# Performance work log

Measured on AMD Instinct MI355X. Metric: run time of the kernel, lower is better.

## Reference

```python
import jax, jax.numpy as jnp
import numpy as np

NX, NY, NM, NDT, NU, ND = 128, 64, 32, 32, 32, 32
N_STEPS, B, TP = 1024, 128, 64


def _spectral_weight(U, sig, V, smin, smax):
    # W = U @ diag(sigma_clamped) @ V with sigma in [smin, smax];
    # spectral (orthogonality) error penalizes non-orthogonal U, V.
    s = smin + (smax - smin) * jax.nn.sigmoid(sig)
    nin, nout = U.shape[0], V.shape[0]
    k = s.shape[0]
    Sigma = jnp.zeros((nin, nout), U.dtype).at[jnp.arange(k), jnp.arange(k)].set(s)
    W = U @ Sigma @ V
    err = jnp.mean((U @ U.T - jnp.eye(nin, dtype=U.dtype)) ** 2) \
        + jnp.mean((V @ V.T - jnp.eye(nout, dtype=V.dtype)) ** 2)
    return W, err


def _pf_weight(w, scal, smin, smax):
    # Perron-Frobenius interval weight: column-stochastic (softmax over rows)
    # scaled elementwise into [smin, smax].
    s = smax - (smax - smin) * jax.nn.sigmoid(scal)
    return s * jax.nn.softmax(w, axis=0)


def setup_inputs() -> dict:
    key = jax.random.key(0)
    ks = jax.random.split(key, 20)
    f = lambda i, sh, sc=1.0: jax.random.normal(ks[i], sh, jnp.float32) * sc
    u = lambda i, sh: jax.random.uniform(ks[i], sh, jnp.float32)
    inp = {
        # forward data args
        "Ym": f(0, (TP, B, NY)),
        "M_flow": u(1, (N_STEPS, B, NM)),
        "DT": u(2, (N_STEPS, B, NDT)),
        "D": u(3, (N_STEPS, B, ND)),
        "XMIN": jnp.zeros((N_STEPS, B, NX), jnp.float32),
        "XMAX": jnp.ones((N_STEPS, B, NX), jnp.float32),
        "UMIN": jnp.zeros((N_STEPS, B, NU), jnp.float32),
        "UMAX": jnp.ones((N_STEPS, B, NU), jnp.float32),
        # learned parameters
        "x0_correct": jnp.zeros((1, NX), jnp.float32),
        "U_A": f(4, (NX, NX), 0.1), "sig_A": u(5, (NX,)), "V_A": f(6, (NX, NX), 0.1),
        "U_C": f(7, (NX, NX), 0.1), "sig_C": u(8, (NY,)), "V_C": f(9, (NY, NY), 0.1),
        "w_E": u(10, (ND, NX)), "s_E": u(11, (ND, NX)),
        "w_B": f(12, (NU, NX), 0.1),
        "W_hf": f(13, (NU, NM, NDT), 0.1),
        "W_ih": f(14, (NY, NX), 0.1), "W_hh": f(15, (NX, NX), 0.1),
        # non-trainable buffers
        "dxmin": -0.5 * jnp.ones((1, NX), jnp.float32),
        "dxmax": 0.5 * jnp.ones((1, NX), jnp.float32),
    }
    return inp


def _forward(Ym, M_flow, DT, D, XMIN, XMAX, UMIN, UMAX, x0_correct,
             U_A, sig_A, V_A, U_C, sig_C, V_C, w_E, s_E, w_B, W_hf,
             W_ih, W_hh, dxmin, dxmax):
    W_A, errA = _spectral_weight(U_A, sig_A, V_A, 0.1, 0.9)   # state transition, sigma in [0.1,0.9]
    W_C, errC = _spectral_weight(U_C, sig_C, V_C, 0.9, 1.0)   # output map, sigma in [0.9,1]
    W_E = _pf_weight(w_E, s_E, 0.05, 1.0)                      # disturbance map
    W_Bpos = jax.nn.relu(w_B)                                  # non-negative input map
    spect_err = errA + errC

    # RNN state estimator over past observations; x0 = last hidden output
    def rnn_step(h, y_t):
        h = jax.nn.gelu(y_t @ W_ih + h @ W_hh)
        return h, None
    h0 = jnp.zeros((Ym.shape[1], W_ih.shape[1]), Ym.dtype)
    x0, _ = jax.lax.scan(rnn_step, h0, Ym)

    def step(x, ins):
        m, dT, d, xmin, xmax, umin, umax = ins
        x_prev = x
        xc = x + x0_correct
        u = jnp.einsum('bi,oij,bj->bo', m, W_hf, dT)   # bilinear heat flow
        Bu = u @ W_Bpos
        Ed = d @ W_E
        x_new = xc @ W_A + Bu + Ed
        y = x_new @ W_C
        sxmin = jax.nn.relu(xmin - x_new)
        sxmax = jax.nn.relu(x_new - xmax)
        sumin = jax.nn.relu(umin - u)
        sumax = jax.nn.relu(u - umax)
        dx_x = x_new - x_prev
        dx_u = jax.nn.relu(dxmin - Bu) + jax.nn.relu(Bu - dxmax)
        dx_d = jax.nn.relu(dxmin - Ed) + jax.nn.relu(Ed - dxmax)
        return x_new, (x_new, y, u, sxmin, sxmax, sumin, sumax, dx_x, dx_u, dx_d)

    _, outs = jax.lax.scan(step, x0, (M_flow, DT, D, XMIN, XMAX, UMIN, UMAX))
    X, Y, U, Sxmin, Sxmax, Sumin, Sumax, Sdx_x, Sdx_u, Sdx_d = outs
    SpectErr = jnp.full((M_flow.shape[0],), spect_err)
    return (X, Y, U, Sxmin, Sxmax, Sumin, Sumax, Sdx_x, Sdx_u, Sdx_d, SpectErr)


def reference(Ym, M_flow, DT, D, XMIN, XMAX, UMIN, UMAX, x0_correct,
              U_A, sig_A, V_A, U_C, sig_C, V_C, w_E, s_E, w_B, W_hf,
              W_ih, W_hh, dxmin, dxmax):
    return _forward(Ym, M_flow, DT, D, XMIN, XMAX, UMIN, UMAX, x0_correct,
                    U_A, sig_A, V_A, U_C, sig_C, V_C, w_E, s_E, w_B, W_hf,
                    W_ih, W_hh, dxmin, dxmax)
```

## Files before the change

kernel.cpp:

```cpp
#include <hip/hip_runtime.h>
#include <math.h>


#define OUT_X      0
#define OUT_Y      16777216
#define OUT_U      25165824
#define OUT_SXMIN  29360128
#define OUT_SXMAX  46137344
#define OUT_SUMIN  62914560
#define OUT_SUMAX  67108864
#define OUT_SDXX   71303168
#define OUT_SDXU   88080384
#define OUT_SDXD   104857600
#define OUT_SPECT  121634816

#define WS_WA     0
#define WS_APOW   65536
#define WS_WC     589824
#define WS_WB     606208
#define WS_WE     614400
#define WS_WHF    622592
#define WS_R      688128
#define WS_ERRP   688640
#define WS_Z      1048576
#define WS_C      5242880
#define WS_XLOC   38797312

#define XSTR 136

typedef _Float16 half8  __attribute__((ext_vector_type(8)));
typedef _Float16 half4v __attribute__((ext_vector_type(4)));
typedef float    floatx4 __attribute__((ext_vector_type(4)));

#define MFMA16(a,b,c) __builtin_amdgcn_mfma_f32_16x16x32_f16((a),(b),(c),0,0,0)

__device__ __forceinline__ float sigm(float x){ return 1.0f/(1.0f+expf(-x)); }
__device__ __forceinline__ float gelu_t(float x){
  float u = 0.7978845608028654f*(x + 0.044715f*x*x*x);
  return 0.5f*x*(1.0f+tanhf(u));
}
__device__ __forceinline__ half8 ldg8h(const float* p){
  const floatx4* p4 = (const floatx4*)p;
  floatx4 a = p4[0], b = p4[1];
  half8 r;
  r[0]=(_Float16)a[0]; r[1]=(_Float16)a[1]; r[2]=(_Float16)a[2]; r[3]=(_Float16)a[3];
  r[4]=(_Float16)b[0]; r[5]=(_Float16)b[1]; r[6]=(_Float16)b[2]; r[7]=(_Float16)b[3];
  return r;
}
__device__ __forceinline__ half8 lds8h(const float* p){
  half8 r;
  #pragma unroll
  for (int e=0;e<8;e++) r[e] = (_Float16)p[e];
  return r;
}
__device__ __forceinline__ floatx4 h4f4(half4v h){
  floatx4 f; f[0]=(float)h[0]; f[1]=(float)h[1]; f[2]=(float)h[2]; f[3]=(float)h[3]; return f;
}
__device__ __forceinline__ half4v f4h4(floatx4 f){
  half4v h; h[0]=(_Float16)f[0]; h[1]=(_Float16)f[1]; h[2]=(_Float16)f[2]; h[3]=(_Float16)f[3]; return h;
}

__global__ __launch_bounds__(256) void k1_weights(
    const float* __restrict__ U_A, const float* __restrict__ sig_A, const float* __restrict__ V_A,
    const float* __restrict__ U_C, const float* __restrict__ sig_C, const float* __restrict__ V_C,
    const float* __restrict__ w_E, const float* __restrict__ s_E,  const float* __restrict__ w_B,
    const float* __restrict__ W_hf, char* __restrict__ ws)
{
  int tid = threadIdx.x, bid = blockIdx.x;
  __shared__ float sA[128];
  __shared__ float sC[64];
  __shared__ float red[256];
  if (tid < 128) sA[tid] = 0.1f + 0.8f*sigm(sig_A[tid]);
  else if (tid < 192) sC[tid-128] = 0.9f + 0.1f*sigm(sig_C[tid-128]);
  __syncthreads();

  float*     wa  = (float*)(ws + WS_WA);
  _Float16*  ap1 = (_Float16*)(ws + WS_APOW);
  _Float16*  wc  = (_Float16*)(ws + WS_WC);
  _Float16*  wb  = (_Float16*)(ws + WS_WB);
  _Float16*  we  = (_Float16*)(ws + WS_WE);
  _Float16*  whf = (_Float16*)(ws + WS_WHF);
  float*     errp= (float*)(ws + WS_ERRP);

  {
    int e = bid*256 + tid;
    int i = e >> 7, j = e & 127;
    float acc = 0.f;
    for (int k=0;k<128;k++) acc += U_A[i*128+k]*sA[k]*V_A[k*128+j];
    wa[i*128+j] = acc;
    ap1[j*128+i] = (_Float16)acc;
  }
  if (bid < 16){
    #pragma unroll
    for (int rep=0;rep<2;rep++){
      int e = bid*512 + rep*256 + tid;
      int i = e >> 6, n = e & 63;
      float acc = 0.f;
      for (int k=0;k<64;k++) acc += U_C[i*128+k]*sC[k]*V_C[k*64+n];
      wc[n*128+i] = (_Float16)acc;
    }
  } else if (bid == 16){
    if (tid < 128){
      int j = tid;
      float mx = -1e30f;
      for (int i=0;i<32;i++) mx = fmaxf(mx, w_E[i*128+j]);
      float ex[32]; float sm = 0.f;
      for (int i=0;i<32;i++){ ex[i] = expf(w_E[i*128+j]-mx); sm += ex[i]; }
      for (int i=0;i<32;i++){
        float s = 1.0f - 0.95f*sigm(s_E[i*128+j]);
        we[j*32+i] = (_Float16)(s*ex[i]/sm);
      }
    }
  } else if (bid == 17){
    if (tid < 128){
      int n = tid;
      for (int k=0;k<32;k++) wb[n*32+k] = (_Float16)fmaxf(w_B[k*128+n], 0.f);
    }
  } else if (bid == 18){
    for (int rep=0;rep<128;rep++){
      int e = rep*256 + tid;
      int o = e >> 10, i = (e>>5)&31, j = e & 31;
      whf[i*1024 + o*32 + j] = (_Float16)W_hf[e];
    }
  }

  float part = 0.f;
  for (int dl = tid; dl < 832; dl += 256){
    int d = bid*832 + dl;
    const float* Mp; int i,j,K,ld; float nrm;
    if (d < 16384){ Mp=U_A; int dd=d;        i=dd>>7; j=dd&127; K=128; ld=128; nrm=16384.f; }
    else if (d < 32768){ Mp=V_A; int dd=d-16384; i=dd>>7; j=dd&127; K=128; ld=128; nrm=16384.f; }
    else if (d < 49152){ Mp=U_C; int dd=d-32768; i=dd>>7; j=dd&127; K=128; ld=128; nrm=16384.f; }
    else { Mp=V_C; int dd=d-49152; i=dd>>6; j=dd&63; K=64; ld=64; nrm=4096.f; }
    float s = 0.f;
    for (int k=0;k<K;k++) s += Mp[i*ld+k]*Mp[j*ld+k];
    float cdf = s - (i==j ? 1.f : 0.f);
    part += cdf*cdf/nrm;
  }
  red[tid] = part;
  __syncthreads();
  for (int off=128; off>0; off>>=1){
    if (tid < off) red[tid] += red[tid+off];
    __syncthreads();
  }
  if (tid == 0) errp[bid] = red[0];
}

__global__ __launch_bounds__(256) void k1b_finalize(
    const float* __restrict__ x0c, char* __restrict__ ws, float* __restrict__ out)
{
  int tid = threadIdx.x;
  const float* errp = (const float*)(ws + WS_ERRP);
  const float* wa   = (const float*)(ws + WS_WA);
  float*       rws  = (float*)(ws + WS_R);
  __shared__ float red[64];
  if (tid < 64) red[tid] = errp[tid];
  __syncthreads();
  if (tid == 0){
    float s = 0.f;
    for (int i=0;i<64;i++) s += red[i];
    red[0] = s;
  }
  __syncthreads();
  float spect = red[0];
  for (int r = tid; r < 1024; r += 256) out[OUT_SPECT + r] = spect;
  if (tid < 128){
    float a = 0.f;
    for (int k=0;k<128;k++) a += x0c[k]*wa[k*128+tid];
    rws[tid] = a;
  }
}

__global__ __launch_bounds__(128,1) void k2_seq(
    const float* __restrict__ Ym, const float* __restrict__ W_ih, const float* __restrict__ W_hh,
    char* __restrict__ ws)
{
  int tid = threadIdx.x, bid = blockIdx.x;
  __shared__ _Float16 xl2[2][64*XSTR];
  __shared__ float yb[64];
  __shared__ float hb[128];

  if (bid < 128){
    int b = bid, j = tid;
    float wih[64], whh[128];
    #pragma unroll
    for (int k=0;k<64;k++)  wih[k] = W_ih[k*128+j];
    #pragma unroll
    for (int k=0;k<128;k++) whh[k] = W_hh[k*128+j];
    hb[j] = 0.f;
    __syncthreads();
    for (int t=0;t<64;t++){
      if (tid < 64) yb[tid] = Ym[(t*128+b)*64 + tid];
      __syncthreads();
      float a = 0.f;
      #pragma unroll
      for (int k=0;k<64;k++)  a += yb[k]*wih[k];
      #pragma unroll
      for (int k=0;k<128;k++) a += hb[k]*whh[k];
      __syncthreads();
      hb[j] = gelu_t(a);
      __syncthreads();
    }
    float* z0 = (float*)(ws + WS_Z);
    z0[b*128 + j] = hb[j];
  } else {
    int wave = tid>>6, lane = tid&63, l15 = lane&15, q = lane>>4;
    const float*    wa = (const float*)(ws + WS_WA);
    const _Float16* a1 = (const _Float16*)(ws + WS_APOW);
    half8 af[4][4];
    #pragma unroll
    for (int mt=0;mt<4;mt++)
      #pragma unroll
      for (int kt=0;kt<4;kt++)
        af[mt][kt] = ldg8h(wa + (wave*64+mt*16+l15)*128 + kt*32 + q*8);
    for (int p=2;p<=16;p++){
      _Float16* dst = (_Float16*)(ws + WS_APOW + (p-1)*32768);
      for (int nt=0;nt<8;nt++){
        floatx4 acc[4];
        #pragma unroll
        for (int mt=0;mt<4;mt++){ acc[mt][0]=0.f; acc[mt][1]=0.f; acc[mt][2]=0.f; acc[mt][3]=0.f; }
        #pragma unroll
        for (int kt=0;kt<4;kt++){
          half8 bf = *(const half8*)(a1 + (nt*16+l15)*128 + kt*32 + q*8);
          #pragma unroll
          for (int mt=0;mt<4;mt++) acc[mt] = MFMA16(af[mt][kt], bf, acc[mt]);
        }
        #pragma unroll
        for (int mt=0;mt<4;mt++){
          half4v hv = f4h4(acc[mt]);
          int mg = wave*64 + mt*16;
          *(half4v*)(dst + (nt*16+l15)*128 + mg + q*4) = hv;
          #pragma unroll
          for (int r=0;r<4;r++) xl2[wave][(mt*16+q*4+r)*XSTR + nt*16+l15] = hv[r];
        }
      }
      #pragma unroll
      for (int mt=0;mt<4;mt++)
        #pragma unroll
        for (int kt=0;kt<4;kt++)
          af[mt][kt] = *(const half8*)(&xl2[wave][(mt*16+l15)*XSTR + kt*32 + q*8]);
    }
  }
}

__global__ __launch_bounds__(256,2) void k3_forcing(
    const float* __restrict__ Mf, const float* __restrict__ pDT, const float* __restrict__ pD,
    const float* __restrict__ pUMIN, const float* __restrict__ pUMAX,
    const float* __restrict__ pdxmin, const float* __restrict__ pdxmax,
    char* __restrict__ ws, float* __restrict__ out)
{
  int t = blockIdx.x, tid = threadIdx.x;
  int wave = tid>>6, lane = tid&63, l15 = lane&15, q = lane>>4;
  __shared__ float mls[128*33];
  __shared__ float uls[4][32*34];
  __shared__ float rls[128], dmn[128], dmx[128];

  const float* rws = (const float*)(ws + WS_R);
  for (int e=tid; e<4096; e+=256){
    float v = Mf[t*4096 + e];
    mls[(e>>5)*33 + (e&31)] = v;
  }
  if (tid < 128){ rls[tid]=rws[tid]; dmn[tid]=pdxmin[tid]; dmx[tid]=pdxmax[tid]; }
  __syncthreads();

  int b0 = wave*32 + l15;
  int b1 = wave*32 + 16 + l15;
  half8 dtf0 = ldg8h(pDT + t*4096 + b0*32 + q*8);
  half8 dtf1 = ldg8h(pDT + t*4096 + b1*32 + q*8);
  half8 ddf0 = ldg8h(pD  + t*4096 + b0*32 + q*8);
  half8 ddf1 = ldg8h(pD  + t*4096 + b1*32 + q*8);

  const _Float16* whf = (const _Float16*)(ws + WS_WHF);
  floatx4 u00,u01,u10,u11;
  u00[0]=u00[1]=u00[2]=u00[3]=0.f; u01=u00; u10=u00; u11=u00;
  for (int i=0;i<32;i++){
    _Float16 m0 = (_Float16)mls[b0*33 + i];
    _Float16 m1 = (_Float16)mls[b1*33 + i];
    half8 a0, a1;
    #pragma unroll
    for (int e=0;e<8;e++){ a0[e] = dtf0[e]*m0; a1[e] = dtf1[e]*m1; }
    half8 bo0 = *(const half8*)(whf + i*1024 + l15*32      + q*8);
    half8 bo1 = *(const half8*)(whf + i*1024 + (16+l15)*32 + q*8);
    u00 = MFMA16(a0, bo0, u00); u01 = MFMA16(a0, bo1, u01);
    u10 = MFMA16(a1, bo0, u10); u11 = MFMA16(a1, bo1, u11);
  }
  #pragma unroll
  for (int mt=0;mt<2;mt++){
    #pragma unroll
    for (int nto=0;nto<2;nto++){
      floatx4 uacc = mt ? (nto?u11:u10) : (nto?u01:u00);
      #pragma unroll
      for (int r=0;r<4;r++){
        int b = wave*32 + mt*16 + q*4 + r;
        int o = nto*16 + l15;
        int ub = t*4096 + b*32 + o;
        float uv = uacc[r];
        out[OUT_U + ub] = uv;
        out[OUT_SUMIN + ub] = fmaxf(pUMIN[ub]-uv, 0.f);
        out[OUT_SUMAX + ub] = fmaxf(uv-pUMAX[ub], 0.f);
        uls[wave][(mt*16+q*4+r)*34 + o] = uv;
      }
    }
  }
  half8 uf0 = lds8h(&uls[wave][(l15)*34 + q*8]);
  half8 uf1 = lds8h(&uls[wave][(16+l15)*34 + q*8]);

  const _Float16* wb = (const _Float16*)(ws + WS_WB);
  const _Float16* we = (const _Float16*)(ws + WS_WE);
  _Float16* cws = (_Float16*)(ws + WS_C);
  for (int nt=0; nt<8; nt++){
    half8 wbf = *(const half8*)(wb + (nt*16+l15)*32 + q*8);
    half8 wef = *(const half8*)(we + (nt*16+l15)*32 + q*8);
    floatx4 zz; zz[0]=zz[1]=zz[2]=zz[3]=0.f;
    floatx4 bu0=MFMA16(uf0, wbf, zz), bu1=MFMA16(uf1, wbf, zz);
    floatx4 ed0=MFMA16(ddf0, wef, zz), ed1=MFMA16(ddf1, wef, zz);
    int col = nt*16 + l15;
    float dn = dmn[col], dxv = dmx[col], rv = rls[col];
    #pragma unroll
    for (int mt=0;mt<2;mt++){
      floatx4 bu = mt?bu1:bu0, ed = mt?ed1:ed0;
      half4v cp;
      #pragma unroll
      for (int r=0;r<4;r++){
        int b = wave*32 + mt*16 + q*4 + r;
        int base = t*16384 + b*128 + col;
        float buv = bu[r], edv = ed[r];
        out[OUT_SDXU + base] = fmaxf(dn-buv,0.f) + fmaxf(buv-dxv,0.f);
        out[OUT_SDXD + base] = fmaxf(dn-edv,0.f) + fmaxf(edv-dxv,0.f);
        cp[r] = (_Float16)(rv + buv + edv);
      }
      *(half4v*)(cws + (((t*8 + (wave*2+mt))*8 + nt)<<8) + lane*4) = cp;
    }
  }
}

__global__ __launch_bounds__(256,1) void k5a_pass1(char* __restrict__ ws)
{
  int tid = threadIdx.x;
  int wave = tid>>6, lane = tid&63, l15 = lane&15, q = lane>>4;
  int chunk = blockIdx.x >> 1, half = blockIdx.x & 1;
  int mt_g = half*4 + wave;
  const _Float16* a1   = (const _Float16*)(ws + WS_APOW);
  const _Float16* cws  = (const _Float16*)(ws + WS_C);
  _Float16*       xloc = (_Float16*)(ws + WS_XLOC);
  __shared__ _Float16 xl[4][16*XSTR];

  half8 bf[8][4];
  #pragma unroll
  for (int nt=0;nt<8;nt++)
    #pragma unroll
    for (int kt=0;kt<4;kt++)
      bf[nt][kt] = *(const half8*)(a1 + (nt*16+l15)*128 + kt*32 + q*8);
  half8 af[4] = {};

  for (int s=0;s<16;s++){
    int t = chunk*16 + s;
    floatx4 acc[8];
    #pragma unroll
    for (int nt=0;nt<8;nt++){
      half4v cv = *(const half4v*)(cws + (((t*8+mt_g)*8+nt)<<8) + lane*4);
      acc[nt] = h4f4(cv);
    }
    #pragma unroll
    for (int kt=0;kt<4;kt++)
      #pragma unroll
      for (int nt=0;nt<8;nt++)
        acc[nt] = MFMA16(af[kt], bf[nt][kt], acc[nt]);
    #pragma unroll
    for (int nt=0;nt<8;nt++){
      half4v hv = f4h4(acc[nt]);
      *(half4v*)(xloc + (((t*8+mt_g)*8+nt)<<8) + lane*4) = hv;
      #pragma unroll
      for (int r=0;r<4;r++) xl[wave][(q*4+r)*XSTR + nt*16+l15] = hv[r];
    }
    #pragma unroll
    for (int kt=0;kt<4;kt++)
      af[kt] = *(const half8*)(&xl[wave][l15*XSTR + kt*32 + q*8]);
  }
}

__global__ __launch_bounds__(64,1) void k5b_boundary(char* __restrict__ ws)
{
  int lane = threadIdx.x, l15 = lane&15, q = lane>>4;
  int mt_g = blockIdx.x;
  const _Float16* a16  = (const _Float16*)(ws + WS_APOW + 15*32768);
  const _Float16* xloc = (const _Float16*)(ws + WS_XLOC);
  float*          z    = (float*)(ws + WS_Z);
  __shared__ _Float16 xl[16*XSTR];

  half8 bf[8][4];
  #pragma unroll
  for (int nt=0;nt<8;nt++)
    #pragma unroll
    for (int kt=0;kt<4;kt++)
      bf[nt][kt] = *(const half8*)(a16 + (nt*16+l15)*128 + kt*32 + q*8);
  half8 af[4];
  #pragma unroll
  for (int kt=0;kt<4;kt++)
    af[kt] = ldg8h(z + (mt_g*16+l15)*128 + kt*32 + q*8);

  for (int c=0;c<63;c++){
    int t = c*16 + 15;
    floatx4 acc[8];
    #pragma unroll
    for (int nt=0;nt<8;nt++){
      half4v hv = *(const half4v*)(xloc + (((t*8+mt_g)*8+nt)<<8) + lane*4);
      acc[nt] = h4f4(hv);
    }
    #pragma unroll
    for (int kt=0;kt<4;kt++)
      #pragma unroll
      for (int nt=0;nt<8;nt++)
        acc[nt] = MFMA16(af[kt], bf[nt][kt], acc[nt]);
    #pragma unroll
    for (int nt=0;nt<8;nt++){
      #pragma unroll
      for (int r=0;r<4;r++){
        int b = mt_g*16 + q*4 + r;
        z[(c+1)*16384 + b*128 + nt*16+l15] = acc[nt][r];
        xl[(q*4+r)*XSTR + nt*16+l15] = (_Float16)acc[nt][r];
      }
    }
    #pragma unroll
    for (int kt=0;kt<4;kt++)
      af[kt] = *(const half8*)(&xl[l15*XSTR + kt*32 + q*8]);
  }
}

__global__ __launch_bounds__(256,2) void k6_epilogue(
    const float* __restrict__ pXMIN, const float* __restrict__ pXMAX,
    char* __restrict__ ws, float* __restrict__ out)
{
  int t = blockIdx.x, tid = threadIdx.x;
  int wave = tid>>6, lane = tid&63, l15 = lane&15, q = lane>>4;
  int c = t>>4, k = t&15;
  __shared__ _Float16 xl[4][32*XSTR];

  const float*    zp   = (const float*)(ws + WS_Z) + c*16384;
  const _Float16* xloc = (const _Float16*)(ws + WS_XLOC);
  const _Float16* ap1  = (const _Float16*)(ws + WS_APOW + k*32768);
  const _Float16* ap0  = (const _Float16*)(ws + WS_APOW + (k-1)*32768);

  half8 zf[2][4];
  #pragma unroll
  for (int mt=0;mt<2;mt++)
    #pragma unroll
    for (int kt=0;kt<4;kt++)
      zf[mt][kt] = ldg8h(zp + (wave*32+mt*16+l15)*128 + kt*32 + q*8);

  for (int nt=0;nt<8;nt++){
    int col = nt*16 + l15;
    floatx4 xt[2], xm[2];
    #pragma unroll
    for (int mt=0;mt<2;mt++)
      xt[mt] = h4f4(*(const half4v*)(xloc + (((t*8 + wave*2+mt)*8 + nt)<<8) + lane*4));
    #pragma unroll
    for (int kt=0;kt<4;kt++){
      half8 b1 = *(const half8*)(ap1 + (nt*16+l15)*128 + kt*32 + q*8);
      #pragma unroll
      for (int mt=0;mt<2;mt++) xt[mt] = MFMA16(zf[mt][kt], b1, xt[mt]);
    }
    if (k > 0){
      #pragma unroll
      for (int mt=0;mt<2;mt++)
        xm[mt] = h4f4(*(const half4v*)(xloc + ((((t-1)*8 + wave*2+mt)*8 + nt)<<8) + lane*4));
      #pragma unroll
      for (int kt=0;kt<4;kt++){
        half8 b0 = *(const half8*)(ap0 + (nt*16+l15)*128 + kt*32 + q*8);
        #pragma unroll
        for (int mt=0;mt<2;mt++) xm[mt] = MFMA16(zf[mt][kt], b0, xm[mt]);
      }
    } else {
      #pragma unroll
      for (int mt=0;mt<2;mt++)
        #pragma unroll
        for (int r=0;r<4;r++)
          xm[mt][r] = zp[(wave*32+mt*16+q*4+r)*128 + col];
    }
    #pragma unroll
    for (int mt=0;mt<2;mt++){
      #pragma unroll
      for (int r=0;r<4;r++){
        int b = wave*32 + mt*16 + q*4 + r;
        int base = t*16384 + b*128 + col;
        float xv = xt[mt][r];
        out[OUT_X + base]     = xv;
        out[OUT_SXMIN + base] = fmaxf(pXMIN[base]-xv, 0.f);
        out[OUT_SXMAX + base] = fmaxf(xv-pXMAX[base], 0.f);
        out[OUT_SDXX + base]  = xv - xm[mt][r];
        xl[wave][(mt*16+q*4+r)*XSTR + col] = (_Float16)xv;
      }
    }
  }
  half8 xf[2][4];
  #pragma unroll
  for (int mt=0;mt<2;mt++)
    #pragma unroll
    for (int kt=0;kt<4;kt++)
      xf[mt][kt] = *(const half8*)(&xl[wave][(mt*16+l15)*XSTR + kt*32 + q*8]);
  const _Float16* wc = (const _Float16*)(ws + WS_WC);
  #pragma unroll
  for (int ny=0;ny<4;ny++){
    floatx4 ya[2];
    ya[0][0]=ya[0][1]=ya[0][2]=ya[0][3]=0.f; ya[1]=ya[0];
    #pragma unroll
    for (int kt=0;kt<4;kt++){
      half8 wcf = *(const half8*)(wc + (ny*16+l15)*128 + kt*32 + q*8);
      #pragma unroll
      for (int mt=0;mt<2;mt++) ya[mt] = MFMA16(xf[mt][kt], wcf, ya[mt]);
    }
    #pragma unroll
    for (int mt=0;mt<2;mt++)
      #pragma unroll
      for (int r=0;r<4;r++){
        int b = wave*32 + mt*16 + q*4 + r;
        out[OUT_Y + t*8192 + b*64 + ny*16+l15] = ya[mt][r];
      }
  }
}

extern "C" void kernel_launch(void* const* d_in, const int* in_sizes, int n_in,
                              void* d_out, int out_size, void* d_ws, size_t ws_size,
                              hipStream_t stream) {
  (void)in_sizes; (void)n_in; (void)out_size; (void)ws_size;
  const float* Ym     = (const float*)d_in[0];
  const float* M_flow = (const float*)d_in[1];
  const float* DT     = (const float*)d_in[2];
  const float* D      = (const float*)d_in[3];
  const float* XMIN   = (const float*)d_in[4];
  const float* XMAX   = (const float*)d_in[5];
  const float* UMIN   = (const float*)d_in[6];
  const float* UMAX   = (const float*)d_in[7];
  const float* x0c    = (const float*)d_in[8];
  const float* U_A    = (const float*)d_in[9];
  const float* sig_A  = (const float*)d_in[10];
  const float* V_A    = (const float*)d_in[11];
  const float* U_C    = (const float*)d_in[12];
  const float* sig_C  = (const float*)d_in[13];
  const float* V_C    = (const float*)d_in[14];
  const float* w_E    = (const float*)d_in[15];
  const float* s_E    = (const float*)d_in[16];
  const float* w_B    = (const float*)d_in[17];
  const float* W_hf   = (const float*)d_in[18];
  const float* W_ih   = (const float*)d_in[19];
  const float* W_hh   = (const float*)d_in[20];
  const float* dxmin  = (const float*)d_in[21];
  const float* dxmax  = (const float*)d_in[22];
  char*  ws  = (char*)d_ws;
  float* out = (float*)d_out;

  hipLaunchKernelGGL(k1_weights, dim3(64), dim3(256), 0, stream,
                     U_A, sig_A, V_A, U_C, sig_C, V_C, w_E, s_E, w_B, W_hf, ws);
  hipLaunchKernelGGL(k1b_finalize, dim3(1), dim3(256), 0, stream, x0c, ws, out);
  hipLaunchKernelGGL(k2_seq, dim3(129), dim3(128), 0, stream, Ym, W_ih, W_hh, ws);
  hipLaunchKernelGGL(k3_forcing, dim3(1024), dim3(256), 0, stream,
                     M_flow, DT, D, UMIN, UMAX, dxmin, dxmax, ws, out);
  hipLaunchKernelGGL(k5a_pass1, dim3(128), dim3(256), 0, stream, ws);
  hipLaunchKernelGGL(k5b_boundary, dim3(8), dim3(64), 0, stream, ws);
  hipLaunchKernelGGL(k6_epilogue, dim3(1024), dim3(256), 0, stream, XMIN, XMAX, ws, out);
}
```

Before: 1.085 ms.

## Merge RNN and power kernels into neighbors, prefetch scans, nontemporal stores

The GRU-like warm-start recurrence moves into extra blocks of the weight kernel, with Ym preloaded into LDS and the hidden state double-buffered so each step needs one barrier instead of three. The A-power computation runs as an extra block of the forcing kernel, removing a launch. The orthogonality error now uses a wave-level dot product with shuffle reductions. k5a is split into one-wave blocks with next-step prefetch of the forcing terms, k5b prefetches boundary states, and the large output writes use nontemporal stores. Together these aim to shorten the serial critical path and launch overhead, at the cost of more LDS use and altered occupancy.

```diff
diff --git a/kernel.cpp b/kernel.cpp
--- a/kernel.cpp
+++ b/kernel.cpp
@@ -60,16 +60,62 @@
   half4v h; h[0]=(_Float16)f[0]; h[1]=(_Float16)f[1]; h[2]=(_Float16)f[2]; h[3]=(_Float16)f[3]; return h;
 }
 
-__global__ __launch_bounds__(256) void k1_weights(
+__global__ __launch_bounds__(256,1) void k1_weights(
     const float* __restrict__ U_A, const float* __restrict__ sig_A, const float* __restrict__ V_A,
     const float* __restrict__ U_C, const float* __restrict__ sig_C, const float* __restrict__ V_C,
     const float* __restrict__ w_E, const float* __restrict__ s_E,  const float* __restrict__ w_B,
-    const float* __restrict__ W_hf, char* __restrict__ ws)
+    const float* __restrict__ W_hf,
+    const float* __restrict__ Ym, const float* __restrict__ W_ih, const float* __restrict__ W_hh,
+    char* __restrict__ ws)
 {
   int tid = threadIdx.x, bid = blockIdx.x;
+
+  if (bid >= 64){
+    int b = bid - 64;
+    __shared__ float ybAll[4096];
+    __shared__ float hbuf[2][128];
+    for (int e=tid; e<4096; e+=256)
+      ybAll[e] = Ym[(e>>6)*8192 + b*64 + (e&63)];
+    if (tid < 128) hbuf[0][tid] = 0.f;
+    float wih[64], whh[128];
+    if (tid < 128){
+      #pragma unroll
+      for (int k=0;k<64;k++)  wih[k] = W_ih[k*128+tid];
+      #pragma unroll
+      for (int k=0;k<128;k++) whh[k] = W_hh[k*128+tid];
+    }
+    __syncthreads();
+    int cur = 0;
+    for (int t=0;t<64;t++){
+      if (tid < 128){
+        const float* yb = &ybAll[t*64];
+        const float* hb = hbuf[cur];
+        float a0=0.f,a1=0.f,a2=0.f,a3=0.f;
+        #pragma unroll
+        for (int k=0;k<64;k+=4){
+          a0 += yb[k]  *wih[k];   a1 += yb[k+1]*wih[k+1];
+          a2 += yb[k+2]*wih[k+2]; a3 += yb[k+3]*wih[k+3];
+        }
+        #pragma unroll
+        for (int k=0;k<128;k+=4){
+          a0 += hb[k]  *whh[k];   a1 += hb[k+1]*whh[k+1];
+          a2 += hb[k+2]*whh[k+2]; a3 += hb[k+3]*whh[k+3];
+        }
+        hbuf[cur^1][tid] = gelu_t((a0+a1)+(a2+a3));
+      }
+      __syncthreads();
+      cur ^= 1;
+    }
+    if (tid < 128){
+      float* z0 = (float*)(ws + WS_Z);
+      z0[b*128 + tid] = hbuf[cur][tid];
+    }
+    return;
+  }
+
   __shared__ float sA[128];
   __shared__ float sC[64];
-  __shared__ float red[256];
+  __shared__ float redw[4];
   if (tid < 128) sA[tid] = 0.1f + 0.8f*sigm(sig_A[tid]);
   else if (tid < 192) sC[tid-128] = 0.9f + 0.1f*sigm(sig_C[tid-128]);
   __syncthreads();
@@ -124,26 +170,34 @@
     }
   }
 
-  float part = 0.f;
-  for (int dl = tid; dl < 832; dl += 256){
-    int d = bid*832 + dl;
-    const float* Mp; int i,j,K,ld; float nrm;
-    if (d < 16384){ Mp=U_A; int dd=d;        i=dd>>7; j=dd&127; K=128; ld=128; nrm=16384.f; }
-    else if (d < 32768){ Mp=V_A; int dd=d-16384; i=dd>>7; j=dd&127; K=128; ld=128; nrm=16384.f; }
-    else if (d < 49152){ Mp=U_C; int dd=d-32768; i=dd>>7; j=dd&127; K=128; ld=128; nrm=16384.f; }
-    else { Mp=V_C; int dd=d-49152; i=dd>>6; j=dd&63; K=64; ld=64; nrm=4096.f; }
-    float s = 0.f;
-    for (int k=0;k<K;k++) s += Mp[i*ld+k]*Mp[j*ld+k];
-    float cdf = s - (i==j ? 1.f : 0.f);
-    part += cdf*cdf/nrm;
-  }
-  red[tid] = part;
+  {
+    int wv = tid>>6, lane = tid&63;
+    float part = 0.f;
+    int dbase = (bid*4 + wv)*208;
+    for (int l=0;l<208;l++){
+      int d = dbase + l;
+      const float* Mp; int i, j, K; float inv;
+      if (d < 16384){ Mp=U_A; i=d>>7; j=d&127; K=128; inv=1.f/16384.f; }
+      else if (d < 32768){ Mp=V_A; int dd=d-16384; i=dd>>7; j=dd&127; K=128; inv=1.f/16384.f; }
+      else if (d < 49152){ Mp=U_C; int dd=d-32768; i=dd>>7; j=dd&127; K=128; inv=1.f/16384.f; }
+      else { Mp=V_C; int dd=d-49152; i=dd>>6; j=dd&63; K=64; inv=1.f/4096.f; }
+      float p;
+      if (K == 128){
+        float2 a = ((const float2*)(Mp + i*128))[lane];
+        float2 b = ((const float2*)(Mp + j*128))[lane];
+        p = a.x*b.x + a.y*b.y;
+      } else {
+        p = Mp[i*64+lane]*Mp[j*64+lane];
+      }
+      #pragma unroll
+      for (int m=1;m<64;m<<=1) p += __shfl_xor(p, m, 64);
+      float cdf = p - (i==j ? 1.f : 0.f);
+      part += cdf*cdf*inv;
+    }
+    if (lane == 0) redw[wv] = part;
+  }
   __syncthreads();
-  for (int off=128; off>0; off>>=1){
-    if (tid < off) red[tid] += red[tid+off];
-    __syncthreads();
-  }
-  if (tid == 0) errp[bid] = red[0];
+  if (tid == 0) errp[bid] = redw[0]+redw[1]+redw[2]+redw[3];
 }
 
 __global__ __launch_bounds__(256) void k1b_finalize(
@@ -171,40 +225,19 @@
   }
 }
 
-__global__ __launch_bounds__(128,1) void k2_seq(
-    const float* __restrict__ Ym, const float* __restrict__ W_ih, const float* __restrict__ W_hh,
-    char* __restrict__ ws)
+__global__ __launch_bounds__(256,2) void k3_forcing(
+    const float* __restrict__ Mf, const float* __restrict__ pDT, const float* __restrict__ pD,
+    const float* __restrict__ pUMIN, const float* __restrict__ pUMAX,
+    const float* __restrict__ pdxmin, const float* __restrict__ pdxmax,
+    char* __restrict__ ws, float* __restrict__ out)
 {
-  int tid = threadIdx.x, bid = blockIdx.x;
-  __shared__ _Float16 xl2[2][64*XSTR];
-  __shared__ float yb[64];
-  __shared__ float hb[128];
-
-  if (bid < 128){
-    int b = bid, j = tid;
-    float wih[64], whh[128];
-    #pragma unroll
-    for (int k=0;k<64;k++)  wih[k] = W_ih[k*128+j];
-    #pragma unroll
-    for (int k=0;k<128;k++) whh[k] = W_hh[k*128+j];
-    hb[j] = 0.f;
-    __syncthreads();
-    for (int t=0;t<64;t++){
-      if (tid < 64) yb[tid] = Ym[(t*128+b)*64 + tid];
-      __syncthreads();
-      float a = 0.f;
-      #pragma unroll
-      for (int k=0;k<64;k++)  a += yb[k]*wih[k];
-      #pragma unroll
-      for (int k=0;k<128;k++) a += hb[k]*whh[k];
-      __syncthreads();
-      hb[j] = gelu_t(a);
-      __syncthreads();
-    }
-    float* z0 = (float*)(ws + WS_Z);
-    z0[b*128 + j] = hb[j];
-  } else {
-    int wave = tid>>6, lane = tid&63, l15 = lane&15, q = lane>>4;
+  int tid = threadIdx.x;
+  int wave = tid>>6, lane = tid&63, l15 = lane&15, q = lane>>4;
+  __shared__ __align__(16) float smemf[8960];
+
+  if (blockIdx.x == 1024){
+    if (tid >= 128) return;
+    _Float16* xl2 = (_Float16*)smemf;
     const float*    wa = (const float*)(ws + WS_WA);
     const _Float16* a1 = (const _Float16*)(ws + WS_APOW);
     half8 af[4][4];
@@ -221,9 +254,9 @@
         for (int mt=0;mt<4;mt++){ acc[mt][0]=0.f; acc[mt][1]=0.f; acc[mt][2]=0.f; acc[mt][3]=0.f; }
         #pragma unroll
         for (int kt=0;kt<4;kt++){
-          half8 bf = *(const half8*)(a1 + (nt*16+l15)*128 + kt*32 + q*8);
+          half8 bfv = *(const half8*)(a1 + (nt*16+l15)*128 + kt*32 + q*8);
           #pragma unroll
-          for (int mt=0;mt<4;mt++) acc[mt] = MFMA16(af[mt][kt], bf, acc[mt]);
+          for (int mt=0;mt<4;mt++) acc[mt] = MFMA16(af[mt][kt], bfv, acc[mt]);
         }
         #pragma unroll
         for (int mt=0;mt<4;mt++){
@@ -231,29 +264,24 @@
           int mg = wave*64 + mt*16;
           *(half4v*)(dst + (nt*16+l15)*128 + mg + q*4) = hv;
           #pragma unroll
-          for (int r=0;r<4;r++) xl2[wave][(mt*16+q*4+r)*XSTR + nt*16+l15] = hv[r];
+          for (int r=0;r<4;r++) xl2[wave*(64*XSTR) + (mt*16+q*4+r)*XSTR + nt*16+l15] = hv[r];
         }
       }
       #pragma unroll
       for (int mt=0;mt<4;mt++)
         #pragma unroll
         for (int kt=0;kt<4;kt++)
-          af[mt][kt] = *(const half8*)(&xl2[wave][(mt*16+l15)*XSTR + kt*32 + q*8]);
-    }
-  }
-}
-
-__global__ __launch_bounds__(256,2) void k3_forcing(
-    const float* __restrict__ Mf, const float* __restrict__ pDT, const float* __restrict__ pD,
-    const float* __restrict__ pUMIN, const float* __restrict__ pUMAX,
-    const float* __restrict__ pdxmin, const float* __restrict__ pdxmax,
-    char* __restrict__ ws, float* __restrict__ out)
-{
-  int t = blockIdx.x, tid = threadIdx.x;
-  int wave = tid>>6, lane = tid&63, l15 = lane&15, q = lane>>4;
-  __shared__ float mls[128*33];
-  __shared__ float uls[4][32*34];
-  __shared__ float rls[128], dmn[128], dmx[128];
+          af[mt][kt] = *(const half8*)(&xl2[wave*(64*XSTR) + (mt*16+l15)*XSTR + kt*32 + q*8]);
+    }
+    return;
+  }
+
+  int t = blockIdx.x;
+  float* mls = smemf;
+  float* uls = smemf + 4224;
+  float* rls = smemf + 8576;
+  float* dmn = smemf + 8704;
+  float* dmx = smemf + 8832;
 
   const float* rws = (const float*)(ws + WS_R);
   for (int e=tid; e<4096; e+=256){
@@ -295,15 +323,15 @@
         int o = nto*16 + l15;
         int ub = t*4096 + b*32 + o;
         float uv = uacc[r];
-        out[OUT_U + ub] = uv;
-        out[OUT_SUMIN + ub] = fmaxf(pUMIN[ub]-uv, 0.f);
-        out[OUT_SUMAX + ub] = fmaxf(uv-pUMAX[ub], 0.f);
-        uls[wave][(mt*16+q*4+r)*34 + o] = uv;
-      }
-    }
-  }
-  half8 uf0 = lds8h(&uls[wave][(l15)*34 + q*8]);
-  half8 uf1 = lds8h(&uls[wave][(16+l15)*34 + q*8]);
+        __builtin_nontemporal_store(uv, &out[OUT_U + ub]);
+        __builtin_nontemporal_store(fmaxf(__builtin_nontemporal_load(&pUMIN[ub])-uv, 0.f), &out[OUT_SUMIN + ub]);
+        __builtin_nontemporal_store(fmaxf(uv-__builtin_nontemporal_load(&pUMAX[ub]), 0.f), &out[OUT_SUMAX + ub]);
+        uls[wave*1088 + (mt*16+q*4+r)*34 + o] = uv;
+      }
+    }
+  }
+  half8 uf0 = lds8h(&uls[wave*1088 + (l15)*34 + q*8]);
+  half8 uf1 = lds8h(&uls[wave*1088 + (16+l15)*34 + q*8]);
 
   const _Float16* wb = (const _Float16*)(ws + WS_WB);
   const _Float16* we = (const _Float16*)(ws + WS_WE);
@@ -325,8 +353,8 @@
         int b = wave*32 + mt*16 + q*4 + r;
         int base = t*16384 + b*128 + col;
         float buv = bu[r], edv = ed[r];
-        out[OUT_SDXU + base] = fmaxf(dn-buv,0.f) + fmaxf(buv-dxv,0.f);
-        out[OUT_SDXD + base] = fmaxf(dn-edv,0.f) + fmaxf(edv-dxv,0.f);
+        __builtin_nontemporal_store(fmaxf(dn-buv,0.f) + fmaxf(buv-dxv,0.f), &out[OUT_SDXU + base]);
+        __builtin_nontemporal_store(fmaxf(dn-edv,0.f) + fmaxf(edv-dxv,0.f), &out[OUT_SDXD + base]);
         cp[r] = (_Float16)(rv + buv + edv);
       }
       *(half4v*)(cws + (((t*8 + (wave*2+mt))*8 + nt)<<8) + lane*4) = cp;
@@ -334,16 +362,14 @@
   }
 }
 
-__global__ __launch_bounds__(256,1) void k5a_pass1(char* __restrict__ ws)
+__global__ __launch_bounds__(64,1) void k5a_pass1(char* __restrict__ ws)
 {
-  int tid = threadIdx.x;
-  int wave = tid>>6, lane = tid&63, l15 = lane&15, q = lane>>4;
-  int chunk = blockIdx.x >> 1, half = blockIdx.x & 1;
-  int mt_g = half*4 + wave;
+  int lane = threadIdx.x, l15 = lane&15, q = lane>>4;
+  int chunk = blockIdx.x >> 3, mt_g = blockIdx.x & 7;
   const _Float16* a1   = (const _Float16*)(ws + WS_APOW);
   const _Float16* cws  = (const _Float16*)(ws + WS_C);
   _Float16*       xloc = (_Float16*)(ws + WS_XLOC);
-  __shared__ _Float16 xl[4][16*XSTR];
+  __shared__ _Float16 xl[16*XSTR];
 
   half8 bf[8][4];
   #pragma unroll
@@ -353,13 +379,21 @@
       bf[nt][kt] = *(const half8*)(a1 + (nt*16+l15)*128 + kt*32 + q*8);
   half8 af[4] = {};
 
+  int t0 = chunk*16;
+  half4v cv[8];
+  #pragma unroll
+  for (int nt=0;nt<8;nt++)
+    cv[nt] = *(const half4v*)(cws + (((t0*8+mt_g)*8+nt)<<8) + lane*4);
+
   for (int s=0;s<16;s++){
-    int t = chunk*16 + s;
+    int t = t0 + s;
     floatx4 acc[8];
     #pragma unroll
-    for (int nt=0;nt<8;nt++){
-      half4v cv = *(const half4v*)(cws + (((t*8+mt_g)*8+nt)<<8) + lane*4);
-      acc[nt] = h4f4(cv);
+    for (int nt=0;nt<8;nt++) acc[nt] = h4f4(cv[nt]);
+    if (s < 15){
+      #pragma unroll
+      for (int nt=0;nt<8;nt++)
+        cv[nt] = *(const half4v*)(cws + ((((t+1)*8+mt_g)*8+nt)<<8) + lane*4);
     }
     #pragma unroll
     for (int kt=0;kt<4;kt++)
@@ -371,11 +405,11 @@
       half4v hv = f4h4(acc[nt]);
       *(half4v*)(xloc + (((t*8+mt_g)*8+nt)<<8) + lane*4) = hv;
       #pragma unroll
-      for (int r=0;r<4;r++) xl[wave][(q*4+r)*XSTR + nt*16+l15] = hv[r];
-    }
-    #pragma unroll
-    for (int kt=0;kt<4;kt++)
-      af[kt] = *(const half8*)(&xl[wave][l15*XSTR + kt*32 + q*8]);
+      for (int r=0;r<4;r++) xl[(q*4+r)*XSTR + nt*16+l15] = hv[r];
+    }
+    #pragma unroll
+    for (int kt=0;kt<4;kt++)
+      af[kt] = *(const half8*)(&xl[l15*XSTR + kt*32 + q*8]);
   }
 }
 
@@ -399,13 +433,20 @@
   for (int kt=0;kt<4;kt++)
     af[kt] = ldg8h(z + (mt_g*16+l15)*128 + kt*32 + q*8);
 
+  half4v pf[8];
+  #pragma unroll
+  for (int nt=0;nt<8;nt++)
+    pf[nt] = *(const half4v*)(xloc + (((15*8+mt_g)*8+nt)<<8) + lane*4);
+
   for (int c=0;c<63;c++){
-    int t = c*16 + 15;
     floatx4 acc[8];
     #pragma unroll
-    for (int nt=0;nt<8;nt++){
-      half4v hv = *(const half4v*)(xloc + (((t*8+mt_g)*8+nt)<<8) + lane*4);
-      acc[nt] = h4f4(hv);
+    for (int nt=0;nt<8;nt++) acc[nt] = h4f4(pf[nt]);
+    if (c < 62){
+      int tn = (c+1)*16 + 15;
+      #pragma unroll
+      for (int nt=0;nt<8;nt++)
+        pf[nt] = *(const half4v*)(xloc + (((tn*8+mt_g)*8+nt)<<8) + lane*4);
     }
     #pragma unroll
     for (int kt=0;kt<4;kt++)
@@ -484,10 +525,10 @@
         int b = wave*32 + mt*16 + q*4 + r;
         int base = t*16384 + b*128 + col;
         float xv = xt[mt][r];
-        out[OUT_X + base]     = xv;
-        out[OUT_SXMIN + base] = fmaxf(pXMIN[base]-xv, 0.f);
-        out[OUT_SXMAX + base] = fmaxf(xv-pXMAX[base], 0.f);
-        out[OUT_SDXX + base]  = xv - xm[mt][r];
+        __builtin_nontemporal_store(xv, &out[OUT_X + base]);
+        __builtin_nontemporal_store(fmaxf(__builtin_nontemporal_load(&pXMIN[base])-xv, 0.f), &out[OUT_SXMIN + base]);
+        __builtin_nontemporal_store(fmaxf(xv-__builtin_nontemporal_load(&pXMAX[base]), 0.f), &out[OUT_SXMAX + base]);
+        __builtin_nontemporal_store(xv - xm[mt][r], &out[OUT_SDXX + base]);
         xl[wave][(mt*16+q*4+r)*XSTR + col] = (_Float16)xv;
       }
     }
@@ -514,7 +555,7 @@
       #pragma unroll
       for (int r=0;r<4;r++){
         int b = wave*32 + mt*16 + q*4 + r;
-        out[OUT_Y + t*8192 + b*64 + ny*16+l15] = ya[mt][r];
+        __builtin_nontemporal_store(ya[mt][r], &out[OUT_Y + t*8192 + b*64 + ny*16+l15]);
       }
   }
 }
@@ -549,13 +590,13 @@
   char*  ws  = (char*)d_ws;
   float* out = (float*)d_out;
 
-  hipLaunchKernelGGL(k1_weights, dim3(64), dim3(256), 0, stream,
-                     U_A, sig_A, V_A, U_C, sig_C, V_C, w_E, s_E, w_B, W_hf, ws);
+  hipLaunchKernelGGL(k1_weights, dim3(192), dim3(256), 0, stream,
+                     U_A, sig_A, V_A, U_C, sig_C, V_C, w_E, s_E, w_B, W_hf,
+                     Ym, W_ih, W_hh, ws);
   hipLaunchKernelGGL(k1b_finalize, dim3(1), dim3(256), 0, stream, x0c, ws, out);
-  hipLaunchKernelGGL(k2_seq, dim3(129), dim3(128), 0, stream, Ym, W_ih, W_hh, ws);
-  hipLaunchKernelGGL(k3_forcing, dim3(1024), dim3(256), 0, stream,
+  hipLaunchKernelGGL(k3_forcing, dim3(1025), dim3(256), 0, stream,
                      M_flow, DT, D, UMIN, UMAX, dxmin, dxmax, ws, out);
-  hipLaunchKernelGGL(k5a_pass1, dim3(128), dim3(256), 0, stream, ws);
+  hipLaunchKernelGGL(k5a_pass1, dim3(512), dim3(64), 0, stream, ws);
   hipLaunchKernelGGL(k5b_boundary, dim3(8), dim3(64), 0, stream, ws);
   hipLaunchKernelGGL(k6_epilogue, dim3(1024), dim3(256), 0, stream, XMIN, XMAX, ws, out);
 }
```

After: 1.036 ms. 4.4% less time.
